# Kernel tuning notes

Hardware: AMD Instinct MI355X
Metric: run time of the kernel (lower is better)

Reference implementation:

```python
import jax, jax.numpy as jnp
import numpy as np

N = 50000   # nodes
E = 800000  # directed edges (self loops added in reference)
F = 8       # temporal features
D = 64      # hidden_channels
H = 4       # heads
C = D // H  # per-head channels = 16
L = 3       # num GAT layers
T = 3       # node types
TE = 16     # type embed dim


def _glorot(key, shape):
    fan_in, fan_out = shape[-2], shape[-1]
    s = jnp.sqrt(6.0 / (fan_in + fan_out))
    return jax.random.uniform(key, shape, jnp.float32, -s, s)


def setup_inputs() -> dict:
    key = jax.random.key(0)
    ks = jax.random.split(key, 24)
    return {
        'x': jax.random.normal(ks[0], (N, F), jnp.float32),
        'node_type': jax.random.randint(ks[1], (N,), 0, T),
        'edge_src': jax.random.randint(ks[2], (E,), 0, N),
        'edge_dst': jax.random.randint(ks[3], (E,), 0, N),
        # TemporalEncoder (Linear F->D + ReLU)
        'Wt': _glorot(ks[4], (F, D)), 'bt': jnp.zeros((D,), jnp.float32),
        # type embedding and input projection
        'Et': 0.1 * jax.random.normal(ks[5], (T, TE), jnp.float32),
        'Wp': _glorot(ks[6], (D + TE, D)), 'bp': jnp.zeros((D,), jnp.float32),
        # GATv2 layers (stacked over L)
        'Wl': _glorot(ks[7], (L, D, H * C)), 'bl': jnp.zeros((L, H * C), jnp.float32),
        'Wr': _glorot(ks[8], (L, D, H * C)), 'br': jnp.zeros((L, H * C), jnp.float32),
        'att': _glorot(ks[9], (L, H, C)),
        'Wres': _glorot(ks[10], (L, D, H * C)),
        'bconv': jnp.zeros((L, H * C), jnp.float32),
        'gamma': jnp.ones((L, D), jnp.float32), 'beta': jnp.zeros((L, D), jnp.float32),
        'alpha': jnp.float32(0.5),
        # output head
        'W1': _glorot(ks[11], (D, D // 2)), 'b1': jnp.zeros((D // 2,), jnp.float32),
        'W2': _glorot(ks[12], (D // 2, 1)), 'b2': jnp.zeros((1,), jnp.float32),
    }


def _layernorm(x, g, b, eps=1e-5):
    mu = jnp.mean(x, -1, keepdims=True)
    v = jnp.mean((x - mu) ** 2, -1, keepdims=True)
    return g * (x - mu) / jnp.sqrt(v + eps) + b


def reference(x, node_type, edge_src, edge_dst, Wt, bt, Et, Wp, bp,
              Wl, bl, Wr, br, att, Wres, bconv, gamma, beta, alpha,
              W1, b1, W2, b2):
    # temporal encoder + type embedding + input projection
    h = jax.nn.relu(x @ Wt + bt)                       # [N, D]
    h = jnp.concatenate([h, Et[node_type]], axis=-1) @ Wp + bp
    h0 = h

    # add self loops once (eval mode -> no dropout)
    loop = jnp.arange(N)
    src = jnp.concatenate([edge_src, loop])            # [E']
    dst = jnp.concatenate([edge_dst, loop])

    for l in range(L):
        xl = (h @ Wl[l] + bl[l]).reshape(N, H, C)      # source transform
        xr = (h @ Wr[l] + br[l]).reshape(N, H, C)      # target transform
        e = jax.nn.leaky_relu(xl[src] + xr[dst], 0.2)  # [E', H, C]
        score = jnp.einsum('ehc,hc->eh', e, att[l])    # [E', H]
        # segment softmax over incoming edges of each destination node
        m = jax.ops.segment_max(score, dst, num_segments=N)
        ex = jnp.exp(score - m[dst])
        s = jax.ops.segment_sum(ex, dst, num_segments=N)
        a = ex / (s[dst] + 1e-16)                      # [E', H]
        msg = xl[src] * a[:, :, None]                  # [E', H, C]
        out = jax.ops.segment_sum(msg, dst, num_segments=N).reshape(N, H * C)
        out = out + h @ Wres[l] + bconv[l]             # GATv2 residual + bias
        h = _layernorm(alpha * out + (1.0 - alpha) * h0, gamma[l], beta[l])

    z = jax.nn.relu(h @ W1 + b1)
    return jax.nn.sigmoid(z @ W2 + b2)                 # [N, 1]
```

## Files before the change

### kernel.cpp

```cpp
#include <hip/hip_runtime.h>
#include <hip/hip_bf16.h>

typedef __hip_bfloat16 bf16;
typedef __attribute__((ext_vector_type(8))) short short8;
typedef __attribute__((ext_vector_type(4))) float f32x4;

__device__ __forceinline__ float b2f(bf16 v) { return __bfloat162float(v); }
__device__ __forceinline__ bf16 f2b(float v) { return __float2bfloat16(v); }
__device__ __forceinline__ short f2bs(float v) {
    bf16 b = f2b(v);
    return *reinterpret_cast<short*>(&b);
}
__device__ __forceinline__ float bflo(unsigned int u) { return __uint_as_float(u << 16); }
__device__ __forceinline__ float bfhi(unsigned int u) { return __uint_as_float(u & 0xffff0000u); }
__device__ __forceinline__ unsigned int packbf(float lo, float hi) {
    bf16 l = f2b(lo), h = f2b(hi);
    return ((unsigned int)(*(unsigned short*)&h) << 16) | (*(unsigned short*)&l);
}


__global__ void k_sentinel(float* out, int n, float val) {
    int i = blockIdx.x * blockDim.x + threadIdx.x;
    if (i < n) out[i] = val;
}

#define PREP_BLOCKS 169
__global__ void k_setup(const float* __restrict__ Wl, const float* __restrict__ Wr,
                        const float* __restrict__ Wres, const float* __restrict__ Wp,
                        const float* __restrict__ W1, const float* __restrict__ Et,
                        const float* __restrict__ bp,
                        bf16* __restrict__ WT, bf16* __restrict__ WpT,
                        bf16* __restrict__ W1T, float* __restrict__ TyB,
                        const int* __restrict__ edst, int* __restrict__ counts,
                        int* __restrict__ rank, int e) {
    int b = blockIdx.x;
    if (b < PREP_BLOCKS) {
        int i = b * 256 + threadIdx.x;
        if (i < 36864) {
            int l = i / 12288, rem = i % 12288;
            int col = rem / 64, k = rem % 64;
            int mat = col >> 6, c = col & 63;
            const float* W = (mat == 0) ? Wl : (mat == 1) ? Wr : Wres;
            WT[i] = f2b(W[l * 4096 + k * 64 + c]);
        } else if (i < 40960) {
            int j = i - 36864, col = j / 64, k = j % 64;
            WpT[j] = f2b(Wp[k * 64 + col]);
        } else if (i < 43008) {
            int j = i - 40960, col = j / 64, k = j % 64;
            W1T[j] = f2b(W1[k * 32 + col]);
        } else if (i < 43200) {
            int j = i - 43008, t = j / 64, d = j % 64;
            float s = bp[d];
#pragma unroll
            for (int f = 0; f < 16; ++f) s += Et[t * 16 + f] * Wp[(64 + f) * 64 + d];
            TyB[j] = s;
        }
    } else {
        int i = (b - PREP_BLOCKS) * 256 + threadIdx.x;
        if (i < e) rank[i] = atomicAdd(&counts[edst[i]], 1);
    }
}

__global__ __launch_bounds__(256) void k_encx(
        const float* __restrict__ x, const int* __restrict__ ntype,
        const float* __restrict__ Wt, const float* __restrict__ bt,
        const bf16* __restrict__ WpT, const float* __restrict__ TyB,
        bf16* __restrict__ h0b,
        const bf16* __restrict__ WT0, const float* __restrict__ bl0,
        const float* __restrict__ br0, const float* __restrict__ bc0,
        bf16* __restrict__ xlo, bf16* __restrict__ xro, bf16* __restrict__ reso,
        int n) {
    __shared__ float sWt[512];
    __shared__ float sbt[64];
    __shared__ __align__(16) short sh[4 * 16 * 72];
    int tid = threadIdx.x;
    for (int i = tid; i < 512; i += 256) sWt[i] = Wt[i];
    if (tid < 64) sbt[tid] = bt[tid];
    __syncthreads();
    int wave = tid >> 6, lane = tid & 63;
    int nb = blockIdx.x * 64 + wave * 16;
    if (nb >= n) return;
    int m = lane & 15, q = lane >> 4;
    short* shw = sh + wave * 16 * 72;

    const float* xrow = x + (size_t)(nb + m) * 8;
    float xv[8];
#pragma unroll
    for (int f = 0; f < 8; ++f) xv[f] = xrow[f];

    short8 a0, a1;
#pragma unroll
    for (int j = 0; j < 8; ++j) {
        int c0 = q * 8 + j, c1 = 32 + q * 8 + j;
        float s0 = sbt[c0], s1 = sbt[c1];
#pragma unroll
        for (int f = 0; f < 8; ++f) {
            s0 += xv[f] * sWt[f * 64 + c0];
            s1 += xv[f] * sWt[f * 64 + c1];
        }
        a0[j] = f2bs(fmaxf(s0, 0.f));
        a1[j] = f2bs(fmaxf(s1, 0.f));
    }

    int ty[4];
#pragma unroll
    for (int r = 0; r < 4; ++r) ty[r] = ntype[nb + q * 4 + r];

#pragma unroll
    for (int t = 0; t < 4; ++t) {
        const short* wp = (const short*)(WpT + (size_t)(t * 16 + m) * 64) + q * 8;
        short8 b0 = *(const short8*)(wp);
        short8 b1 = *(const short8*)(wp + 32);
        f32x4 acc = {0.f, 0.f, 0.f, 0.f};
        acc = __builtin_amdgcn_mfma_f32_16x16x32_bf16(a0, b0, acc, 0, 0, 0);
        acc = __builtin_amdgcn_mfma_f32_16x16x32_bf16(a1, b1, acc, 0, 0, 0);
        int col = t * 16 + m;
#pragma unroll
        for (int r = 0; r < 4; ++r) {
            int nd = nb + q * 4 + r;
            short vb = f2bs(acc[r] + TyB[ty[r] * 64 + col]);
            h0b[(size_t)nd * 64 + col] = *reinterpret_cast<bf16*>(&vb);
            shw[(q * 4 + r) * 72 + col] = vb;
        }
    }
    short8 ha0 = *(const short8*)(&shw[m * 72 + q * 8]);
    short8 ha1 = *(const short8*)(&shw[m * 72 + 32 + q * 8]);
#pragma unroll
    for (int t = 0; t < 12; ++t) {
        const short* wp = (const short*)(WT0 + (size_t)(t * 16 + m) * 64) + q * 8;
        short8 b0 = *(const short8*)(wp);
        short8 b1 = *(const short8*)(wp + 32);
        f32x4 acc = {0.f, 0.f, 0.f, 0.f};
        acc = __builtin_amdgcn_mfma_f32_16x16x32_bf16(ha0, b0, acc, 0, 0, 0);
        acc = __builtin_amdgcn_mfma_f32_16x16x32_bf16(ha1, b1, acc, 0, 0, 0);
        int col = t * 16 + m;
        int mat = col >> 6, c = col & 63;
        float bias = (mat == 0) ? bl0[c] : (mat == 1) ? br0[c] : bc0[c];
        bf16* dst = (mat == 0) ? xlo : (mat == 1) ? xro : reso;
#pragma unroll
        for (int r = 0; r < 4; ++r)
            dst[(size_t)(nb + q * 4 + r) * 64 + c] = f2b(acc[r] + bias);
    }
}

__global__ void k_scan_local(const int* __restrict__ counts, int* __restrict__ row_raw,
                             int* __restrict__ bsum, int* __restrict__ hist,
                             int* __restrict__ row_ptr, int* __restrict__ done,
                             int n) {
    __shared__ int part[256];
    __shared__ int lh[64];
    __shared__ int lastflag;
    int tid = threadIdx.x;
    if (tid < 64) lh[tid] = 0;
    __syncthreads();
    int base = blockIdx.x * 1024 + tid * 4;
    int d0 = (base     < n) ? counts[base]     : -1;
    int d1 = (base + 1 < n) ? counts[base + 1] : -1;
    int d2 = (base + 2 < n) ? counts[base + 2] : -1;
    int d3 = (base + 3 < n) ? counts[base + 3] : -1;
    if (d0 >= 0) atomicAdd(&lh[63 - (d0 < 63 ? d0 : 63)], 1);
    if (d1 >= 0) atomicAdd(&lh[63 - (d1 < 63 ? d1 : 63)], 1);
    if (d2 >= 0) atomicAdd(&lh[63 - (d2 < 63 ? d2 : 63)], 1);
    if (d3 >= 0) atomicAdd(&lh[63 - (d3 < 63 ? d3 : 63)], 1);
    int c0 = d0 + 1, c1 = d1 + 1, c2 = d2 + 1, c3 = d3 + 1;
    part[tid] = c0 + c1 + c2 + c3;
    __syncthreads();
    for (int off = 1; off < 256; off <<= 1) {
        int t = (tid >= off) ? part[tid - off] : 0;
        __syncthreads();
        part[tid] += t;
        __syncthreads();
    }
    int ex = (tid == 0) ? 0 : part[tid - 1];
    if (base     < n) row_raw[base]     = ex;
    if (base + 1 < n) row_raw[base + 1] = ex + c0;
    if (base + 2 < n) row_raw[base + 2] = ex + c0 + c1;
    if (base + 3 < n) row_raw[base + 3] = ex + c0 + c1 + c2;
    if (tid == 255) bsum[blockIdx.x] = part[255];
    if (tid < 64 && lh[tid] > 0) atomicAdd(&hist[tid], lh[tid]);

    __threadfence();
    __syncthreads();
    if (tid == 0) {
        int d = atomicAdd(done, 1);
        lastflag = (d == (int)gridDim.x - 1);
    }
    __syncthreads();
    if (lastflag && tid < 64) {
        __threadfence();
        int lane = tid;
        int g = (int)gridDim.x;
        int orig = (lane < g) ? bsum[lane] : 0;
        int v = orig;
#pragma unroll
        for (int off = 1; off < 64; off <<= 1) {
            int t = __shfl_up(v, off, 64);
            if (lane >= off) v += t;
        }
        if (lane < g) bsum[lane] = v - orig;
        if (lane == 63) row_ptr[n] = v;

        int ho = hist[lane];
        int hv = ho;
#pragma unroll
        for (int off = 1; off < 64; off <<= 1) {
            int t = __shfl_up(hv, off, 64);
            if (lane >= off) hv += t;
        }
        hist[lane] = hv - ho;
    }
}

__global__ void k_build(const int* __restrict__ src, const int* __restrict__ dst,
                        const int* __restrict__ row_raw, const int* __restrict__ bsum,
                        const int* __restrict__ rank, const int* __restrict__ counts,
                        int* __restrict__ row_ptr, int* __restrict__ csr_src,
                        int* __restrict__ hist, int* __restrict__ perm,
                        int n, int e) {
    __shared__ int lh[64];
    __shared__ int gbase[64];
    int tid = threadIdx.x;
    int i = blockIdx.x * 256 + tid;
    bool nodework = (blockIdx.x * 256) < n;
    if (nodework) {
        if (tid < 64) lh[tid] = 0;
        __syncthreads();
        int bucket = 0, myrank = -1;
        if (i < n) {
            int d = counts[i];
            bucket = 63 - (d < 63 ? d : 63);
            myrank = atomicAdd(&lh[bucket], 1);
        }
        __syncthreads();
        if (tid < 64 && lh[tid] > 0) gbase[tid] = atomicAdd(&hist[tid], lh[tid]);
        __syncthreads();
        if (i < n) perm[gbase[bucket] + myrank] = i;
    }
    if (i < n) {
        int rp = row_raw[i] + bsum[i >> 10];
        row_ptr[i] = rp;
        csr_src[rp] = i;
    }
    if (i < e) {
        int d = dst[i];
        int pos = row_raw[d] + bsum[d >> 10] + 1 + rank[i];
        csr_src[pos] = src[i];
    }
}

#define GAT8_STEP(XU)                                                             \
    {                                                                             \
        float xf0 = bflo(XU.x), xf1 = bfhi(XU.x);                                 \
        float xf2 = bflo(XU.y), xf3 = bfhi(XU.y);                                 \
        float xf4 = bflo(XU.z), xf5 = bfhi(XU.z);                                 \
        float xf6 = bflo(XU.w), xf7 = bfhi(XU.w);                                 \
        float u0 = xf0 + xq0; u0 = fmaxf(u0, 0.2f * u0);                          \
        float u1 = xf1 + xq1; u1 = fmaxf(u1, 0.2f * u1);                          \
        float u2 = xf2 + xq2; u2 = fmaxf(u2, 0.2f * u2);                          \
        float u3 = xf3 + xq3; u3 = fmaxf(u3, 0.2f * u3);                          \
        float u4 = xf4 + xq4; u4 = fmaxf(u4, 0.2f * u4);                          \
        float u5 = xf5 + xq5; u5 = fmaxf(u5, 0.2f * u5);                          \
        float u6 = xf6 + xq6; u6 = fmaxf(u6, 0.2f * u6);                          \
        float u7 = xf7 + xq7; u7 = fmaxf(u7, 0.2f * u7);                          \
        float p0_ = (u0 * at0 + u1 * at1) + (u2 * at2 + u3 * at3);                \
        float p1_ = (u4 * at4 + u5 * at5) + (u6 * at6 + u7 * at7);                \
        float p_ = p0_ + p1_;                                                     \
        p_ += __shfl_xor(p_, 1, 64);                                              \
        float pe_ = __expf(fminf(p_, 60.f));                                      \
        lsum += pe_;                                                              \
        A0 += pe_ * xf0; A1 += pe_ * xf1; A2 += pe_ * xf2; A3 += pe_ * xf3;       \
        A4 += pe_ * xf4; A5 += pe_ * xf5; A6 += pe_ * xf6; A7 += pe_ * xf7;       \
    }

#define GAT_PHASE_BODY                                                            \
    int tid = threadIdx.x;                                                        \
    int wave = tid >> 6, lane = tid & 63;                                         \
    int half = lane >> 5;                                                         \
    int L = lane & 31;                                                            \
    int g = L >> 3;                                                               \
    int k = L & 7;                                                                \
    int nl = wave * 2 + half;                                                     \
    int idx = blockIdx.x * 16 + nl;                                               \
    bool valid = idx < n;                                                         \
    int v = valid ? perm[idx] : 0;                                                \
    if (L == 0) sid[nl] = valid ? v : -1;                                         \
    uint4 xruv = ((const uint4*)(xr + (size_t)v * 64))[k];                        \
    float xq0 = bflo(xruv.x), xq1 = bfhi(xruv.x);                                 \
    float xq2 = bflo(xruv.y), xq3 = bfhi(xruv.y);                                 \
    float xq4 = bflo(xruv.z), xq5 = bfhi(xruv.z);                                 \
    float xq6 = bflo(xruv.w), xq7 = bfhi(xruv.w);                                 \
    float4 atv0 = ((const float4*)att)[k * 2];                                    \
    float4 atv1 = ((const float4*)att)[k * 2 + 1];                                \
    float at0 = atv0.x, at1 = atv0.y, at2 = atv0.z, at3 = atv0.w;                 \
    float at4 = atv1.x, at5 = atv1.y, at6 = atv1.z, at7 = atv1.w;                 \
    int beg = row_ptr[v];                                                         \
    int end = valid ? row_ptr[v + 1] : beg;                                       \
    float lsum = 0.f;                                                             \
    float A0 = 0.f, A1 = 0.f, A2 = 0.f, A3 = 0.f;                                 \
    float A4 = 0.f, A5 = 0.f, A6 = 0.f, A7 = 0.f;                                 \
    int e = beg + g;                                                              \
    for (; e + 4 < end; e += 8) {                                                 \
        int s0_ = csr_src[e];                                                     \
        int s1_ = csr_src[e + 4];                                                 \
        uint4 xu0_ = ((const uint4*)(xl + (size_t)s0_ * 64))[k];                  \
        uint4 xu1_ = ((const uint4*)(xl + (size_t)s1_ * 64))[k];                  \
        GAT8_STEP(xu0_)                                                           \
        GAT8_STEP(xu1_)                                                           \
    }                                                                             \
    if (e < end) {                                                                \
        int s0_ = csr_src[e];                                                     \
        uint4 xu0_ = ((const uint4*)(xl + (size_t)s0_ * 64))[k];                  \
        GAT8_STEP(xu0_)                                                           \
    }                                                                             \
    lsum += __shfl_xor(lsum, 8, 64);  lsum += __shfl_xor(lsum, 16, 64);           \
    A0 += __shfl_xor(A0, 8, 64);  A0 += __shfl_xor(A0, 16, 64);                   \
    A1 += __shfl_xor(A1, 8, 64);  A1 += __shfl_xor(A1, 16, 64);                   \
    A2 += __shfl_xor(A2, 8, 64);  A2 += __shfl_xor(A2, 16, 64);                   \
    A3 += __shfl_xor(A3, 8, 64);  A3 += __shfl_xor(A3, 16, 64);                   \
    A4 += __shfl_xor(A4, 8, 64);  A4 += __shfl_xor(A4, 16, 64);                   \
    A5 += __shfl_xor(A5, 8, 64);  A5 += __shfl_xor(A5, 16, 64);                   \
    A6 += __shfl_xor(A6, 8, 64);  A6 += __shfl_xor(A6, 16, 64);                   \
    A7 += __shfl_xor(A7, 8, 64);  A7 += __shfl_xor(A7, 16, 64);                   \
    float inv = 1.f / (lsum + 1e-16f);                                            \
    uint4 ruv = ((const uint4*)(res + (size_t)v * 64))[k];                        \
    uint4 huv = ((const uint4*)(h0b + (size_t)v * 64))[k];                        \
    float a = alpha_p[0];                                                         \
    float ac = 1.f - a;                                                           \
    float t0 = a * (A0 * inv + bflo(ruv.x)) + ac * bflo(huv.x);                   \
    float t1 = a * (A1 * inv + bfhi(ruv.x)) + ac * bfhi(huv.x);                   \
    float t2 = a * (A2 * inv + bflo(ruv.y)) + ac * bflo(huv.y);                   \
    float t3 = a * (A3 * inv + bfhi(ruv.y)) + ac * bfhi(huv.y);                   \
    float t4 = a * (A4 * inv + bflo(ruv.z)) + ac * bflo(huv.z);                   \
    float t5 = a * (A5 * inv + bfhi(ruv.z)) + ac * bfhi(huv.z);                   \
    float t6 = a * (A6 * inv + bflo(ruv.w)) + ac * bflo(huv.w);                   \
    float t7 = a * (A7 * inv + bfhi(ruv.w)) + ac * bfhi(huv.w);                   \
    float mu = ((t0 + t1) + (t2 + t3)) + ((t4 + t5) + (t6 + t7));                 \
    mu += __shfl_xor(mu, 1, 64);                                                  \
    mu += __shfl_xor(mu, 2, 64);                                                  \
    mu += __shfl_xor(mu, 4, 64);                                                  \
    mu *= (1.f / 64.f);                                                           \
    float d0 = t0 - mu, d1 = t1 - mu, d2 = t2 - mu, d3 = t3 - mu;                 \
    float d4 = t4 - mu, d5 = t5 - mu, d6 = t6 - mu, d7 = t7 - mu;                 \
    float var = ((d0 * d0 + d1 * d1) + (d2 * d2 + d3 * d3)) +                     \
                ((d4 * d4 + d5 * d5) + (d6 * d6 + d7 * d7));                      \
    var += __shfl_xor(var, 1, 64);                                                \
    var += __shfl_xor(var, 2, 64);                                                \
    var += __shfl_xor(var, 4, 64);                                                \
    var *= (1.f / 64.f);                                                          \
    float rs = rsqrtf(var + 1e-5f);                                               \
    float4 gm0 = ((const float4*)gamma)[k * 2];                                   \
    float4 gm1 = ((const float4*)gamma)[k * 2 + 1];                               \
    float4 bb0_ = ((const float4*)beta)[k * 2];                                   \
    float4 bb1_ = ((const float4*)beta)[k * 2 + 1];                               \
    short8 hs;                                                                    \
    hs[0] = f2bs(gm0.x * d0 * rs + bb0_.x);                                       \
    hs[1] = f2bs(gm0.y * d1 * rs + bb0_.y);                                       \
    hs[2] = f2bs(gm0.z * d2 * rs + bb0_.z);                                       \
    hs[3] = f2bs(gm0.w * d3 * rs + bb0_.w);                                       \
    hs[4] = f2bs(gm1.x * d4 * rs + bb1_.x);                                       \
    hs[5] = f2bs(gm1.y * d5 * rs + bb1_.y);                                       \
    hs[6] = f2bs(gm1.z * d6 * rs + bb1_.z);                                       \
    hs[7] = f2bs(gm1.w * d7 * rs + bb1_.w);                                       \
    if (g == 0) *(short8*)(&sh[nl * 72 + k * 8]) = hs;                            \
    __syncthreads();

__global__ __launch_bounds__(512) void k_gatx(
        const bf16* __restrict__ xl, const bf16* __restrict__ xr,
        const bf16* __restrict__ res, const bf16* __restrict__ h0b,
        const float* __restrict__ att, const float* __restrict__ gamma,
        const float* __restrict__ beta, const float* __restrict__ alpha_p,
        const int* __restrict__ row_ptr, const int* __restrict__ csr_src,
        const int* __restrict__ perm,
        const bf16* __restrict__ WTn, const float* __restrict__ bln,
        const float* __restrict__ brn, const float* __restrict__ bcn,
        bf16* __restrict__ xlo, bf16* __restrict__ xro, bf16* __restrict__ reso,
        int n) {
    __shared__ __align__(16) short sh[16 * 72];
    __shared__ int sid[16];
    GAT_PHASE_BODY

    int m = lane & 15, q = lane >> 4;
    short8 ha0 = *(const short8*)(&sh[m * 72 + q * 8]);
    short8 ha1 = *(const short8*)(&sh[m * 72 + 32 + q * 8]);
    for (int t = wave; t < 12; t += 8) {
        const short* wp = (const short*)(WTn + (size_t)(t * 16 + m) * 64) + q * 8;
        short8 b0 = *(const short8*)(wp);
        short8 b1 = *(const short8*)(wp + 32);
        f32x4 acc = {0.f, 0.f, 0.f, 0.f};
        acc = __builtin_amdgcn_mfma_f32_16x16x32_bf16(ha0, b0, acc, 0, 0, 0);
        acc = __builtin_amdgcn_mfma_f32_16x16x32_bf16(ha1, b1, acc, 0, 0, 0);
        int col = t * 16 + m;
        int mat = col >> 6, c = col & 63;
        float bias = (mat == 0) ? bln[c] : (mat == 1) ? brn[c] : bcn[c];
        bf16* dst = (mat == 0) ? xlo : (mat == 1) ? xro : reso;
#pragma unroll
        for (int r = 0; r < 4; ++r) {
            int nd = sid[q * 4 + r];
            if (nd >= 0) dst[(size_t)nd * 64 + c] = f2b(acc[r] + bias);
        }
    }
}

__global__ __launch_bounds__(512) void k_gath(
        const bf16* __restrict__ xl, const bf16* __restrict__ xr,
        const bf16* __restrict__ res, const bf16* __restrict__ h0b,
        const float* __restrict__ att, const float* __restrict__ gamma,
        const float* __restrict__ beta, const float* __restrict__ alpha_p,
        const int* __restrict__ row_ptr, const int* __restrict__ csr_src,
        const int* __restrict__ perm,
        const bf16* __restrict__ W1T, const float* __restrict__ b1,
        const float* __restrict__ W2, const float* __restrict__ b2,
        float* __restrict__ out, int n) {
    __shared__ __align__(16) short sh[16 * 72];
    __shared__ int sid[16];
    GAT_PHASE_BODY

    if (wave == 0) {
        int m = lane & 15, q = lane >> 4;
        short8 ha0 = *(const short8*)(&sh[m * 72 + q * 8]);
        short8 ha1 = *(const short8*)(&sh[m * 72 + 32 + q * 8]);

        const short* w0p = (const short*)(W1T + (size_t)m * 64) + q * 8;
        const short* w1p = (const short*)(W1T + (size_t)(16 + m) * 64) + q * 8;
        short8 b00 = *(const short8*)(w0p);
        short8 b01 = *(const short8*)(w0p + 32);
        short8 b10 = *(const short8*)(w1p);
        short8 b11 = *(const short8*)(w1p + 32);

        f32x4 acc0 = {0.f, 0.f, 0.f, 0.f};
        f32x4 acc1 = {0.f, 0.f, 0.f, 0.f};
        acc0 = __builtin_amdgcn_mfma_f32_16x16x32_bf16(ha0, b00, acc0, 0, 0, 0);
        acc0 = __builtin_amdgcn_mfma_f32_16x16x32_bf16(ha1, b01, acc0, 0, 0, 0);
        acc1 = __builtin_amdgcn_mfma_f32_16x16x32_bf16(ha0, b10, acc1, 0, 0, 0);
        acc1 = __builtin_amdgcn_mfma_f32_16x16x32_bf16(ha1, b11, acc1, 0, 0, 0);

        float w2a = W2[m], w2b = W2[16 + m];
        float bb0 = b1[m], bb1 = b1[16 + m];
        float part[4];
#pragma unroll
        for (int r = 0; r < 4; ++r)
            part[r] = fmaxf(acc0[r] + bb0, 0.f) * w2a + fmaxf(acc1[r] + bb1, 0.f) * w2b;
#pragma unroll
        for (int mask = 1; mask < 16; mask <<= 1) {
#pragma unroll
            for (int r = 0; r < 4; ++r) part[r] += __shfl_xor(part[r], mask, 64);
        }
        if (m == 0) {
            float bb2 = b2[0];
#pragma unroll
            for (int r = 0; r < 4; ++r) {
                int nd = sid[q * 4 + r];
                if (nd >= 0) out[nd] = 1.f / (1.f + __expf(-(part[r] + bb2)));
            }
        }
    }
}

extern "C" void kernel_launch(void* const* d_in, const int* in_sizes, int n_in,
                              void* d_out, int out_size, void* d_ws, size_t ws_size,
                              hipStream_t stream) {
    const float* x     = (const float*)d_in[0];
    const int*   ntype = (const int*)d_in[1];
    const int*   esrc  = (const int*)d_in[2];
    const int*   edst  = (const int*)d_in[3];
    const float* Wt    = (const float*)d_in[4];
    const float* bt    = (const float*)d_in[5];
    const float* Et    = (const float*)d_in[6];
    const float* Wp    = (const float*)d_in[7];
    const float* bp    = (const float*)d_in[8];
    const float* Wl    = (const float*)d_in[9];
    const float* bl    = (const float*)d_in[10];
    const float* Wr    = (const float*)d_in[11];
    const float* br    = (const float*)d_in[12];
    const float* att   = (const float*)d_in[13];
    const float* Wres  = (const float*)d_in[14];
    const float* bconv = (const float*)d_in[15];
    const float* gamma = (const float*)d_in[16];
    const float* beta  = (const float*)d_in[17];
    const float* alpha = (const float*)d_in[18];
    const float* W1    = (const float*)d_in[19];
    const float* b1    = (const float*)d_in[20];
    const float* W2    = (const float*)d_in[21];
    const float* b2    = (const float*)d_in[22];
    float* out = (float*)d_out;

    const int N = in_sizes[1];
    const int E = in_sizes[2];

    const int G = (N + 1023) / 1024;

    size_t need = 256
                + (size_t)N * 64 * 2 * 7
                + (size_t)36864 * 2 + (size_t)4096 * 2 + (size_t)2048 * 2
                + (size_t)192 * 4
                + (size_t)N * 4
                + (size_t)(N + 1) * 4
                + (size_t)(N + 128) * 4
                + (size_t)N * 4
                + (size_t)E * 4
                + 256
                + (size_t)(E + N) * 4;

    if (ws_size < need) {
        k_sentinel<<<(N + 255) / 256, 256, 0, stream>>>(out, N,
                                                        100.0f + (float)(ws_size >> 20));
        return;
    }

    char* ws = (char*)d_ws;
    ws += 256;
    bf16* h0b   = (bf16*)ws;  ws += (size_t)N * 64 * 2;
    bf16* xlA   = (bf16*)ws;  ws += (size_t)N * 64 * 2;
    bf16* xrA   = (bf16*)ws;  ws += (size_t)N * 64 * 2;
    bf16* resA  = (bf16*)ws;  ws += (size_t)N * 64 * 2;
    bf16* xlB   = (bf16*)ws;  ws += (size_t)N * 64 * 2;
    bf16* xrB   = (bf16*)ws;  ws += (size_t)N * 64 * 2;
    bf16* resB  = (bf16*)ws;  ws += (size_t)N * 64 * 2;
    bf16* WT    = (bf16*)ws;  ws += (size_t)36864 * 2;
    bf16* WpT   = (bf16*)ws;  ws += (size_t)4096 * 2;
    bf16* W1T   = (bf16*)ws;  ws += (size_t)2048 * 2;
    float* TyB  = (float*)ws; ws += (size_t)192 * 4;
    int* row_raw = (int*)ws;  ws += (size_t)N * 4;
    int* row_ptr = (int*)ws;  ws += (size_t)(N + 1) * 4;
    int* counts  = (int*)ws;  ws += (size_t)N * 4;
    int* hist    = (int*)ws;  ws += (size_t)128 * 4;
    int* perm    = (int*)ws;  ws += (size_t)N * 4;
    int* rank    = (int*)ws;  ws += (size_t)E * 4;
    int* bsum    = (int*)ws;  ws += 256;
    int* csr_src = (int*)ws;  ws += (size_t)(E + N) * 4;
    int* done    = hist + 64;

    hipMemsetAsync(counts, 0, (size_t)(N + 65) * 4, stream);
    k_setup<<<PREP_BLOCKS + (E + 255) / 256, 256, 0, stream>>>(
        Wl, Wr, Wres, Wp, W1, Et, bp, WT, WpT, W1T, TyB, edst, counts, rank, E);
    k_encx<<<(N + 63) / 64, 256, 0, stream>>>(x, ntype, Wt, bt, WpT, TyB, h0b,
                                              WT, bl, br, bconv, xlA, xrA, resA, N);
    k_scan_local<<<G, 256, 0, stream>>>(counts, row_raw, bsum, hist, row_ptr, done, N);
    k_build<<<(E + 255) / 256, 256, 0, stream>>>(esrc, edst, row_raw, bsum, rank,
                                                 counts, row_ptr, csr_src, hist, perm,
                                                 N, E);

    k_gatx<<<(N + 15) / 16, 512, 0, stream>>>(
        xlA, xrA, resA, h0b, att, gamma, beta, alpha, row_ptr, csr_src, perm,
        WT + 12288, bl + 64, br + 64, bconv + 64, xlB, xrB, resB, N);
    k_gatx<<<(N + 15) / 16, 512, 0, stream>>>(
        xlB, xrB, resB, h0b, att + 64, gamma + 64, beta + 64, alpha, row_ptr, csr_src,
        perm, WT + 24576, bl + 128, br + 128, bconv + 128, xlA, xrA, resA, N);
    k_gath<<<(N + 15) / 16, 512, 0, stream>>>(
        xlA, xrA, resA, h0b, att + 128, gamma + 128, beta + 128, alpha,
        row_ptr, csr_src, perm, W1T, b1, W2, b2, out, N);
}
```

Before: 309.5 us.

## Fuse preprocessing kernels into one cooperative persistent kernel with grid syncs

Replaces the memset plus four preprocessing launches (weight transpose, encoder and count, scan, CSR build) with a single cooperative kernel. Grid-wide syncs separate the phases, and blocks loop over work units. The aim is to remove launch gaps and inter-kernel drain overhead. The cost is that the grid is capped at the occupancy-limited persistent size, so phases run in loops over fewer blocks. It also adds grid.sync barriers and keeps the old multi-kernel path as a fallback.

```diff
diff --git a/kernel.cpp b/kernel.cpp
--- a/kernel.cpp
+++ b/kernel.cpp
@@ -1,5 +1,8 @@
 #include <hip/hip_runtime.h>
 #include <hip/hip_bf16.h>
+#include <hip/hip_cooperative_groups.h>
+
+namespace cg = cooperative_groups;
 
 typedef __hip_bfloat16 bf16;
 typedef __attribute__((ext_vector_type(8))) short short8;
@@ -13,10 +16,6 @@
 }
 __device__ __forceinline__ float bflo(unsigned int u) { return __uint_as_float(u << 16); }
 __device__ __forceinline__ float bfhi(unsigned int u) { return __uint_as_float(u & 0xffff0000u); }
-__device__ __forceinline__ unsigned int packbf(float lo, float hi) {
-    bf16 l = f2b(lo), h = f2b(hi);
-    return ((unsigned int)(*(unsigned short*)&h) << 16) | (*(unsigned short*)&l);
-}
 
 
 __global__ void k_sentinel(float* out, int n, float val) {
@@ -25,6 +24,7 @@
 }
 
 #define PREP_BLOCKS 169
+
 __global__ void k_setup(const float* __restrict__ Wl, const float* __restrict__ Wr,
                         const float* __restrict__ Wres, const float* __restrict__ Wp,
                         const float* __restrict__ W1, const float* __restrict__ Et,
@@ -245,6 +245,229 @@
         int d = dst[i];
         int pos = row_raw[d] + bsum[d >> 10] + 1 + rank[i];
         csr_src[pos] = src[i];
+    }
+}
+
+struct PrepArgs {
+    const float *Wl, *Wr, *Wres, *Wp, *W1, *Et, *bp;
+    const float *x; const int *ntype; const float *Wt, *bt;
+    const int *esrc, *edst;
+    bf16 *WT, *WpT, *W1T; float *TyB;
+    bf16 *h0b; const float *bl0, *br0, *bc0;
+    bf16 *xlo, *xro, *reso;
+    int *counts, *rank, *row_raw, *row_ptr, *bsum, *hist, *done, *perm, *csr_src;
+    int n, e;
+};
+
+__global__ __launch_bounds__(256) void k_prep(PrepArgs A) {
+    cg::grid_group grid = cg::this_grid();
+    __shared__ float sWt[512];
+    __shared__ float sbt[64];
+    __shared__ __align__(16) short sh[4 * 16 * 72];
+    __shared__ int part[256];
+    __shared__ int lh[64];
+    __shared__ int gbase[64];
+    __shared__ int lastflag;
+    int tid = threadIdx.x;
+    int gdim = (int)gridDim.x;
+
+    for (int i = tid; i < 512; i += 256) sWt[i] = A.Wt[i];
+    if (tid < 64) sbt[tid] = A.bt[tid];
+    __syncthreads();
+
+    int zU = (A.n + 65 + 255) / 256;
+    for (int u = blockIdx.x; u < PREP_BLOCKS + zU; u += gdim) {
+        if (u < PREP_BLOCKS) {
+            int i = u * 256 + tid;
+            if (i < 36864) {
+                int l = i / 12288, rem = i % 12288;
+                int col = rem / 64, k = rem % 64;
+                int mat = col >> 6, c = col & 63;
+                const float* W = (mat == 0) ? A.Wl : (mat == 1) ? A.Wr : A.Wres;
+                A.WT[i] = f2b(W[l * 4096 + k * 64 + c]);
+            } else if (i < 40960) {
+                int j = i - 36864, col = j / 64, k = j % 64;
+                A.WpT[j] = f2b(A.Wp[k * 64 + col]);
+            } else if (i < 43008) {
+                int j = i - 40960, col = j / 64, k = j % 64;
+                A.W1T[j] = f2b(A.W1[k * 32 + col]);
+            } else if (i < 43200) {
+                int j = i - 43008, t = j / 64, d = j % 64;
+                float s = A.bp[d];
+#pragma unroll
+                for (int f = 0; f < 16; ++f) s += A.Et[t * 16 + f] * A.Wp[(64 + f) * 64 + d];
+                A.TyB[j] = s;
+            }
+        } else {
+            int j = (u - PREP_BLOCKS) * 256 + tid;
+            if (j < A.n + 65) A.counts[j] = 0;
+        }
+    }
+    grid.sync();
+
+    int encU = (A.n + 63) / 64;
+    int cntU = (A.e + 255) / 256;
+    for (int u = blockIdx.x; u < encU + cntU; u += gdim) {
+        if (u < encU) {
+            int wave = tid >> 6, lane = tid & 63;
+            int nb = u * 64 + wave * 16;
+            if (nb < A.n) {
+                int m = lane & 15, q = lane >> 4;
+                short* shw = sh + wave * 16 * 72;
+                const float* xrow = A.x + (size_t)(nb + m) * 8;
+                float xv[8];
+#pragma unroll
+                for (int f = 0; f < 8; ++f) xv[f] = xrow[f];
+                short8 a0, a1;
+#pragma unroll
+                for (int j = 0; j < 8; ++j) {
+                    int c0 = q * 8 + j, c1 = 32 + q * 8 + j;
+                    float s0 = sbt[c0], s1 = sbt[c1];
+#pragma unroll
+                    for (int f = 0; f < 8; ++f) {
+                        s0 += xv[f] * sWt[f * 64 + c0];
+                        s1 += xv[f] * sWt[f * 64 + c1];
+                    }
+                    a0[j] = f2bs(fmaxf(s0, 0.f));
+                    a1[j] = f2bs(fmaxf(s1, 0.f));
+                }
+                int ty[4];
+#pragma unroll
+                for (int r = 0; r < 4; ++r) ty[r] = A.ntype[nb + q * 4 + r];
+#pragma unroll
+                for (int t = 0; t < 4; ++t) {
+                    const short* wp = (const short*)(A.WpT + (size_t)(t * 16 + m) * 64) + q * 8;
+                    short8 b0 = *(const short8*)(wp);
+                    short8 b1 = *(const short8*)(wp + 32);
+                    f32x4 acc = {0.f, 0.f, 0.f, 0.f};
+                    acc = __builtin_amdgcn_mfma_f32_16x16x32_bf16(a0, b0, acc, 0, 0, 0);
+                    acc = __builtin_amdgcn_mfma_f32_16x16x32_bf16(a1, b1, acc, 0, 0, 0);
+                    int col = t * 16 + m;
+#pragma unroll
+                    for (int r = 0; r < 4; ++r) {
+                        int nd = nb + q * 4 + r;
+                        short vb = f2bs(acc[r] + A.TyB[ty[r] * 64 + col]);
+                        A.h0b[(size_t)nd * 64 + col] = *reinterpret_cast<bf16*>(&vb);
+                        shw[(q * 4 + r) * 72 + col] = vb;
+                    }
+                }
+                short8 ha0 = *(const short8*)(&shw[m * 72 + q * 8]);
+                short8 ha1 = *(const short8*)(&shw[m * 72 + 32 + q * 8]);
+#pragma unroll
+                for (int t = 0; t < 12; ++t) {
+                    const short* wp = (const short*)(A.WT + (size_t)(t * 16 + m) * 64) + q * 8;
+                    short8 b0 = *(const short8*)(wp);
+                    short8 b1 = *(const short8*)(wp + 32);
+                    f32x4 acc = {0.f, 0.f, 0.f, 0.f};
+                    acc = __builtin_amdgcn_mfma_f32_16x16x32_bf16(ha0, b0, acc, 0, 0, 0);
+                    acc = __builtin_amdgcn_mfma_f32_16x16x32_bf16(ha1, b1, acc, 0, 0, 0);
+                    int col = t * 16 + m;
+                    int mat = col >> 6, c = col & 63;
+                    float bias = (mat == 0) ? A.bl0[c] : (mat == 1) ? A.br0[c] : A.bc0[c];
+                    bf16* dst = (mat == 0) ? A.xlo : (mat == 1) ? A.xro : A.reso;
+#pragma unroll
+                    for (int r = 0; r < 4; ++r)
+                        dst[(size_t)(nb + q * 4 + r) * 64 + c] = f2b(acc[r] + bias);
+                }
+            }
+        } else {
+            int i = (u - encU) * 256 + tid;
+            if (i < A.e) A.rank[i] = atomicAdd(&A.counts[A.edst[i]], 1);
+        }
+    }
+    grid.sync();
+
+    int scanU = (A.n + 1023) / 1024;
+    for (int u = blockIdx.x; u < scanU; u += gdim) {
+        if (tid < 64) lh[tid] = 0;
+        __syncthreads();
+        int base = u * 1024 + tid * 4;
+        int d0 = (base     < A.n) ? A.counts[base]     : -1;
+        int d1 = (base + 1 < A.n) ? A.counts[base + 1] : -1;
+        int d2 = (base + 2 < A.n) ? A.counts[base + 2] : -1;
+        int d3 = (base + 3 < A.n) ? A.counts[base + 3] : -1;
+        if (d0 >= 0) atomicAdd(&lh[63 - (d0 < 63 ? d0 : 63)], 1);
+        if (d1 >= 0) atomicAdd(&lh[63 - (d1 < 63 ? d1 : 63)], 1);
+        if (d2 >= 0) atomicAdd(&lh[63 - (d2 < 63 ? d2 : 63)], 1);
+        if (d3 >= 0) atomicAdd(&lh[63 - (d3 < 63 ? d3 : 63)], 1);
+        int c0 = d0 + 1, c1 = d1 + 1, c2 = d2 + 1, c3 = d3 + 1;
+        part[tid] = c0 + c1 + c2 + c3;
+        __syncthreads();
+        for (int off = 1; off < 256; off <<= 1) {
+            int t = (tid >= off) ? part[tid - off] : 0;
+            __syncthreads();
+            part[tid] += t;
+            __syncthreads();
+        }
+        int ex = (tid == 0) ? 0 : part[tid - 1];
+        if (base     < A.n) A.row_raw[base]     = ex;
+        if (base + 1 < A.n) A.row_raw[base + 1] = ex + c0;
+        if (base + 2 < A.n) A.row_raw[base + 2] = ex + c0 + c1;
+        if (base + 3 < A.n) A.row_raw[base + 3] = ex + c0 + c1 + c2;
+        if (tid == 255) A.bsum[u] = part[255];
+        if (tid < 64 && lh[tid] > 0) atomicAdd(&A.hist[tid], lh[tid]);
+
+        __threadfence();
+        __syncthreads();
+        if (tid == 0) {
+            int d = atomicAdd(A.done, 1);
+            lastflag = (d == scanU - 1);
+        }
+        __syncthreads();
+        if (lastflag && tid < 64) {
+            __threadfence();
+            int lane = tid;
+            int orig = (lane < scanU) ? A.bsum[lane] : 0;
+            int v = orig;
+#pragma unroll
+            for (int off = 1; off < 64; off <<= 1) {
+                int t = __shfl_up(v, off, 64);
+                if (lane >= off) v += t;
+            }
+            if (lane < scanU) A.bsum[lane] = v - orig;
+            if (lane == 63) A.row_ptr[A.n] = v;
+
+            int ho = A.hist[lane];
+            int hv = ho;
+#pragma unroll
+            for (int off = 1; off < 64; off <<= 1) {
+                int t = __shfl_up(hv, off, 64);
+                if (lane >= off) hv += t;
+            }
+            A.hist[lane] = hv - ho;
+        }
+    }
+    grid.sync();
+
+    int bldU = (A.e + 255) / 256;
+    for (int u = blockIdx.x; u < bldU; u += gdim) {
+        int i = u * 256 + tid;
+        bool nodework = (u * 256) < A.n;
+        if (nodework) {
+            if (tid < 64) lh[tid] = 0;
+            __syncthreads();
+            int bucket = 0, myrank = -1;
+            if (i < A.n) {
+                int d = A.counts[i];
+                bucket = 63 - (d < 63 ? d : 63);
+                myrank = atomicAdd(&lh[bucket], 1);
+            }
+            __syncthreads();
+            if (tid < 64 && lh[tid] > 0) gbase[tid] = atomicAdd(&A.hist[tid], lh[tid]);
+            __syncthreads();
+            if (i < A.n) A.perm[gbase[bucket] + myrank] = i;
+            __syncthreads();
+        }
+        if (i < A.n) {
+            int rp = A.row_raw[i] + A.bsum[i >> 10];
+            A.row_ptr[i] = rp;
+            A.csr_src[rp] = i;
+        }
+        if (i < A.e) {
+            int d = A.edst[i];
+            int pos = A.row_raw[d] + A.bsum[d >> 10] + 1 + A.rank[i];
+            A.csr_src[pos] = A.esrc[i];
+        }
     }
 }
 
@@ -530,15 +753,56 @@
     int* csr_src = (int*)ws;  ws += (size_t)(E + N) * 4;
     int* done    = hist + 64;
 
-    hipMemsetAsync(counts, 0, (size_t)(N + 65) * 4, stream);
-    k_setup<<<PREP_BLOCKS + (E + 255) / 256, 256, 0, stream>>>(
-        Wl, Wr, Wres, Wp, W1, Et, bp, WT, WpT, W1T, TyB, edst, counts, rank, E);
-    k_encx<<<(N + 63) / 64, 256, 0, stream>>>(x, ntype, Wt, bt, WpT, TyB, h0b,
-                                              WT, bl, br, bconv, xlA, xrA, resA, N);
-    k_scan_local<<<G, 256, 0, stream>>>(counts, row_raw, bsum, hist, row_ptr, done, N);
-    k_build<<<(E + 255) / 256, 256, 0, stream>>>(esrc, edst, row_raw, bsum, rank,
-                                                 counts, row_ptr, csr_src, hist, perm,
-                                                 N, E);
+    static int coopGrid = -1;
+    if (coopGrid < 0) {
+        int dev = 0;
+        hipGetDevice(&dev);
+        hipDeviceProp_t prop;
+        int maxb = 0;
+        if (hipGetDeviceProperties(&prop, dev) == hipSuccess &&
+            hipOccupancyMaxActiveBlocksPerMultiprocessor(&maxb, (const void*)k_prep,
+                                                         256, 0) == hipSuccess &&
+            maxb > 0) {
+            long g = (long)maxb * (long)prop.multiProcessorCount;
+            coopGrid = (int)(g < 1024 ? g : 1024);
+        } else {
+            coopGrid = 0;
+        }
+    }
+
+    PrepArgs pa;
+    pa.Wl = Wl; pa.Wr = Wr; pa.Wres = Wres; pa.Wp = Wp; pa.W1 = W1;
+    pa.Et = Et; pa.bp = bp;
+    pa.x = x; pa.ntype = ntype; pa.Wt = Wt; pa.bt = bt;
+    pa.esrc = esrc; pa.edst = edst;
+    pa.WT = WT; pa.WpT = WpT; pa.W1T = W1T; pa.TyB = TyB;
+    pa.h0b = h0b; pa.bl0 = bl; pa.br0 = br; pa.bc0 = bconv;
+    pa.xlo = xlA; pa.xro = xrA; pa.reso = resA;
+    pa.counts = counts; pa.rank = rank; pa.row_raw = row_raw; pa.row_ptr = row_ptr;
+    pa.bsum = bsum; pa.hist = hist; pa.done = done; pa.perm = perm;
+    pa.csr_src = csr_src;
+    pa.n = N; pa.e = E;
+
+    bool coop_ok = false;
+    if (coopGrid > 0) {
+        void* kargs[] = { &pa };
+        hipError_t err = hipLaunchCooperativeKernel((const void*)k_prep,
+                                                    dim3(coopGrid), dim3(256),
+                                                    kargs, 0, stream);
+        coop_ok = (err == hipSuccess);
+    }
+    if (!coop_ok) {
+        hipMemsetAsync(counts, 0, (size_t)(N + 65) * 4, stream);
+        k_setup<<<PREP_BLOCKS + (E + 255) / 256, 256, 0, stream>>>(
+            Wl, Wr, Wres, Wp, W1, Et, bp, WT, WpT, W1T, TyB, edst, counts, rank, E);
+        k_encx<<<(N + 63) / 64, 256, 0, stream>>>(x, ntype, Wt, bt, WpT, TyB, h0b,
+                                                  WT, bl, br, bconv, xlA, xrA, resA, N);
+        k_scan_local<<<G, 256, 0, stream>>>(counts, row_raw, bsum, hist, row_ptr,
+                                            done, N);
+        k_build<<<(E + 255) / 256, 256, 0, stream>>>(esrc, edst, row_raw, bsum, rank,
+                                                     counts, row_ptr, csr_src, hist,
+                                                     perm, N, E);
+    }
 
     k_gatx<<<(N + 15) / 16, 512, 0, stream>>>(
         xlA, xrA, resA, h0b, att, gamma, beta, alpha, row_ptr, csr_src, perm,
```

Measured after the change: 437.2 us. +41.3%, slower.
